# Kernel tuning notes

Measured on AMD Instinct MI355X. Metric: run time of the kernel, lower is better.

Reference implementation:

```python
import jax, jax.numpy as jnp
import numpy as np

B, C, H, W = 8, 64, 256, 256  # dim=64 -> chunks 32/16/8/8

def _dwconv3x3(x, w, b):
    # x: [N,Cg,H,W], w: [Cg,1,3,3] depthwise
    y = jax.lax.conv_general_dilated(
        x, w, window_strides=(1, 1), padding=((1, 1), (1, 1)),
        feature_group_count=x.shape[1],
        dimension_numbers=('NCHW', 'OIHW', 'NCHW'))
    return y + b[None, :, None, None]

def _maxpool4(x):
    # exact 4x4/stride-4 max pool == adaptive_max_pool2d when sizes divide
    return jax.lax.reduce_window(x, -jnp.inf, jax.lax.max,
                                 (1, 1, 4, 4), (1, 1, 4, 4), 'VALID')

def _upnearest(x, s):
    # nearest interpolate to (H,W) from (H/s,W/s) == repeat by s
    return jnp.repeat(jnp.repeat(x, s, axis=2), s, axis=3)

def setup_inputs() -> dict:
    key = jax.random.key(0)
    ks = jax.random.split(key, 11)
    sc = 0.05
    return {
        'x':  jax.random.normal(ks[0], (B, C, H, W), jnp.float32),
        'w1': jax.random.normal(ks[1], (32, 1, 3, 3), jnp.float32) * sc,
        'b1': jax.random.normal(ks[2], (32,), jnp.float32) * sc,
        'w2': jax.random.normal(ks[3], (16, 1, 3, 3), jnp.float32) * sc,
        'b2': jax.random.normal(ks[4], (16,), jnp.float32) * sc,
        'w3': jax.random.normal(ks[5], (8, 1, 3, 3), jnp.float32) * sc,
        'b3': jax.random.normal(ks[6], (8,), jnp.float32) * sc,
        'w4': jax.random.normal(ks[7], (8, 1, 3, 3), jnp.float32) * sc,
        'b4': jax.random.normal(ks[8], (8,), jnp.float32) * sc,
        'wa': jax.random.normal(ks[9], (64, 64), jnp.float32) * sc,  # 1x1 conv
        'ba': jax.random.normal(ks[10], (64,), jnp.float32) * sc,
    }

def reference(x, w1, b1, w2, b2, w3, b3, w4, b4, wa, ba):
    c = x.shape[1]
    xa, xb = x[:, : c // 2], x[:, c // 2 :]            # 32 / 32 channels
    x1 = _dwconv3x3(xa, w1, b1)                        # [B,32,H,W]
    p2 = _maxpool4(xb)                                 # [B,32,H/4,W/4]
    p2a, p2b = p2[:, :16], p2[:, 16:]
    x2 = _upnearest(_dwconv3x3(p2a, w2, b2), 4)        # [B,16,H,W]
    p3 = _maxpool4(p2b)                                # [B,16,H/16,W/16]
    p3a, p3b = p3[:, :8], p3[:, 8:]
    x3 = _upnearest(_dwconv3x3(p3a, w3, b3), 16)       # [B,8,H,W]
    p4 = _maxpool4(p3b)                                # [B,8,H/64,W/64]
    x4 = _upnearest(_dwconv3x3(p4, w4, b4), 64)        # [B,8,H,W]
    cat = jnp.concatenate([x1, x2, x3, x4], axis=1)    # [B,64,H,W]
    agg = jnp.einsum('oc,bchw->bohw', wa, cat) + ba[None, :, None, None]
    return jax.nn.gelu(agg, approximate=False) * x
```

## Files before the change

### kernel.cpp

```cpp
#include <hip/hip_runtime.h>
#include <math.h>

#define NB 8
#define NC 64
#define NH 256
#define NW 256

typedef short short8 __attribute__((ext_vector_type(8)));
typedef float f32x4 __attribute__((ext_vector_type(4)));

__device__ __forceinline__ unsigned short f2bf(float f) {
    unsigned int u = __float_as_uint(f);
    u += 0x7FFFu + ((u >> 16) & 1u);
    return (unsigned short)(u >> 16);
}

__device__ __forceinline__ int slot_of(int px, int g) {
    return g ^ (px & 7) ^ ((px >> 3) & 7);
}

__launch_bounds__(256)
__global__ void pyramid_kernel(const float* __restrict__ x,
                               const float* __restrict__ w2, const float* __restrict__ b2,
                               const float* __restrict__ w3, const float* __restrict__ b3,
                               const float* __restrict__ w4, const float* __restrict__ b4,
                               float* __restrict__ x2c, float* __restrict__ x3c,
                               float* __restrict__ x4c) {
    __shared__ float pl[64 * 65];
    __shared__ float pl2[16 * 17];
    __shared__ float pl3[16];

    const int tid = threadIdx.x;
    const int c = blockIdx.x & 31;
    const int b = blockIdx.x >> 5;
    const size_t plane = (size_t)NH * NW;
    const float* src = x + ((size_t)(b * 64 + 32 + c)) * plane;

#pragma unroll
    for (int i = 0; i < 16; ++i) {
        int o = tid + 256 * i;
        int pw = o & 63, ph = o >> 6;
        const float* s2 = src + (size_t)(ph * 4) * NW + pw * 4;
        float m = -INFINITY;
#pragma unroll
        for (int r = 0; r < 4; ++r) {
            float4 v = *reinterpret_cast<const float4*>(s2 + (size_t)r * NW);
            m = fmaxf(m, fmaxf(fmaxf(v.x, v.y), fmaxf(v.z, v.w)));
        }
        pl[ph * 65 + pw] = m;
    }
    __syncthreads();

    if (c < 16) {
        float* dst = x2c + ((size_t)(b * 16 + c)) * 4096;
        const float* wc = w2 + c * 9;
        float bb = b2[c];
#pragma unroll
        for (int i = 0; i < 16; ++i) {
            int o = tid + 256 * i;
            int pw = o & 63, ph = o >> 6;
            float acc = bb;
#pragma unroll
            for (int dy = -1; dy <= 1; ++dy) {
                int yy = ph + dy;
                if (yy < 0 || yy >= 64) continue;
#pragma unroll
                for (int dx = -1; dx <= 1; ++dx) {
                    int xx = pw + dx;
                    if (xx < 0 || xx >= 64) continue;
                    acc += pl[yy * 65 + xx] * wc[(dy + 1) * 3 + (dx + 1)];
                }
            }
            dst[o] = acc;
        }
    } else {
        {
            int pw = tid & 15, ph = tid >> 4;
            float m = -INFINITY;
#pragma unroll
            for (int r = 0; r < 4; ++r)
#pragma unroll
                for (int cc = 0; cc < 4; ++cc)
                    m = fmaxf(m, pl[(ph * 4 + r) * 65 + pw * 4 + cc]);
            pl2[ph * 17 + pw] = m;
        }
        __syncthreads();
        if (c < 24) {
            int pw = tid & 15, ph = tid >> 4;
            const float* wc = w3 + (c - 16) * 9;
            float acc = b3[c - 16];
#pragma unroll
            for (int dy = -1; dy <= 1; ++dy) {
                int yy = ph + dy;
                if (yy < 0 || yy >= 16) continue;
#pragma unroll
                for (int dx = -1; dx <= 1; ++dx) {
                    int xx = pw + dx;
                    if (xx < 0 || xx >= 16) continue;
                    acc += pl2[yy * 17 + xx] * wc[(dy + 1) * 3 + (dx + 1)];
                }
            }
            x3c[((size_t)(b * 8 + (c - 16))) * 256 + tid] = acc;
        } else {
            if (tid < 16) {
                int pw = tid & 3, ph = tid >> 2;
                float m = -INFINITY;
#pragma unroll
                for (int r = 0; r < 4; ++r)
#pragma unroll
                    for (int cc = 0; cc < 4; ++cc)
                        m = fmaxf(m, pl2[(ph * 4 + r) * 17 + pw * 4 + cc]);
                pl3[ph * 4 + pw] = m;
            }
            __syncthreads();
            if (tid < 16) {
                int pw = tid & 3, ph = tid >> 2;
                const float* wc = w4 + (c - 24) * 9;
                float acc = b4[c - 24];
#pragma unroll
                for (int dy = -1; dy <= 1; ++dy) {
                    int yy = ph + dy;
                    if (yy < 0 || yy >= 4) continue;
#pragma unroll
                    for (int dx = -1; dx <= 1; ++dx) {
                        int xx = pw + dx;
                        if (xx < 0 || xx >= 4) continue;
                        acc += pl3[yy * 4 + xx] * wc[(dy + 1) * 3 + (dx + 1)];
                    }
                }
                x4c[((size_t)(b * 8 + (c - 24))) * 16 + tid] = acc;
            }
        }
    }
}

__launch_bounds__(256)
__global__ void fused_main(const float* __restrict__ x,
                           const float* __restrict__ w1, const float* __restrict__ b1,
                           const float* __restrict__ x2c,
                           const float* __restrict__ x3c,
                           const float* __restrict__ x4c,
                           const float* __restrict__ wa, const float* __restrict__ ba,
                           float* __restrict__ out) {
    __shared__ __align__(16) unsigned short cat_lds[256 * 64];
    __shared__ __align__(16) unsigned short wa_lds[64 * 64];

    const int tid = threadIdx.x;
    const int q = tid & 63;
    const int cg = tid >> 6;
    const int h = blockIdx.x & 255;
    const int b = blockIdx.x >> 8;
    const size_t plane = (size_t)NH * NW;
    const float* xb = x + (size_t)b * NC * plane;

    {
        int r = tid >> 2;
        int g0 = (tid & 3) * 2;
#pragma unroll
        for (int gg = 0; gg < 2; ++gg) {
            int g = g0 + gg;
            const float* srcw = wa + r * 64 + g * 8;
            int4 pk;
            pk.x = (unsigned)f2bf(srcw[0]) | ((unsigned)f2bf(srcw[1]) << 16);
            pk.y = (unsigned)f2bf(srcw[2]) | ((unsigned)f2bf(srcw[3]) << 16);
            pk.z = (unsigned)f2bf(srcw[4]) | ((unsigned)f2bf(srcw[5]) << 16);
            pk.w = (unsigned)f2bf(srcw[6]) | ((unsigned)f2bf(srcw[7]) << 16);
            *reinterpret_cast<int4*>(&wa_lds[r * 64 + slot_of(r, g) * 8]) = pk;
        }
    }

    const bool hv0 = (h > 0), hv2 = (h < NH - 1);
    const int hm = hv0 ? h - 1 : h;
    const int hp = hv2 ? h + 1 : h;
    float conv[8][4];
#pragma unroll
    for (int j = 0; j < 8; ++j) {
        const int c = cg * 8 + j;
        const float* srcc = xb + (size_t)c * plane;
        float4 a0 = *reinterpret_cast<const float4*>(srcc + (size_t)hm * NW + 4 * q);
        float4 a1 = *reinterpret_cast<const float4*>(srcc + (size_t)h  * NW + 4 * q);
        float4 a2 = *reinterpret_cast<const float4*>(srcc + (size_t)hp * NW + 4 * q);
        const float* wc = w1 + c * 9;
        float k0 = hv0 ? wc[0] : 0.f, k1 = hv0 ? wc[1] : 0.f, k2 = hv0 ? wc[2] : 0.f;
        float k3 = wc[3], k4 = wc[4], k5 = wc[5];
        float k6 = hv2 ? wc[6] : 0.f, k7 = hv2 ? wc[7] : 0.f, k8 = hv2 ? wc[8] : 0.f;
        float p0 = __shfl_up(a0.w, 1), p1 = __shfl_up(a1.w, 1), p2 = __shfl_up(a2.w, 1);
        float n0 = __shfl_down(a0.x, 1), n1 = __shfl_down(a1.x, 1), n2 = __shfl_down(a2.x, 1);
        if (q == 0)  { p0 = 0.f; p1 = 0.f; p2 = 0.f; }
        if (q == 63) { n0 = 0.f; n1 = 0.f; n2 = 0.f; }
        float r0[6] = {p0, a0.x, a0.y, a0.z, a0.w, n0};
        float r1[6] = {p1, a1.x, a1.y, a1.z, a1.w, n1};
        float r2[6] = {p2, a2.x, a2.y, a2.z, a2.w, n2};
#pragma unroll
        for (int i = 0; i < 4; ++i) {
            conv[j][i] = k0 * r0[i] + k1 * r0[i + 1] + k2 * r0[i + 2]
                       + k3 * r1[i] + k4 * r1[i + 1] + k5 * r1[i + 2]
                       + k6 * r2[i] + k7 * r2[i + 1] + k8 * r2[i + 2]
                       + b1[c];
        }
    }
#pragma unroll
    for (int i = 0; i < 4; ++i) {
        int px = 4 * q + i;
        int4 pk;
        pk.x = (unsigned)f2bf(conv[0][i]) | ((unsigned)f2bf(conv[1][i]) << 16);
        pk.y = (unsigned)f2bf(conv[2][i]) | ((unsigned)f2bf(conv[3][i]) << 16);
        pk.z = (unsigned)f2bf(conv[4][i]) | ((unsigned)f2bf(conv[5][i]) << 16);
        pk.w = (unsigned)f2bf(conv[6][i]) | ((unsigned)f2bf(conv[7][i]) << 16);
        *reinterpret_cast<int4*>(&cat_lds[px * 64 + slot_of(px, cg) * 8]) = pk;
    }

    {
        float pv[8];
        const int h4 = h >> 2, h16 = h >> 4, h64 = h >> 6;
        if (cg == 0) {
#pragma unroll
            for (int j = 0; j < 8; ++j)
                pv[j] = x2c[(((size_t)b * 16 + j) * 64 + h4) * 64 + q];
        } else if (cg == 1) {
#pragma unroll
            for (int j = 0; j < 8; ++j)
                pv[j] = x2c[(((size_t)b * 16 + 8 + j) * 64 + h4) * 64 + q];
        } else if (cg == 2) {
#pragma unroll
            for (int j = 0; j < 8; ++j)
                pv[j] = x3c[(((size_t)b * 8 + j) * 16 + h16) * 16 + (q >> 2)];
        } else {
#pragma unroll
            for (int j = 0; j < 8; ++j)
                pv[j] = x4c[(((size_t)b * 8 + j) * 4 + h64) * 4 + (q >> 4)];
        }
        int4 pk;
        pk.x = (unsigned)f2bf(pv[0]) | ((unsigned)f2bf(pv[1]) << 16);
        pk.y = (unsigned)f2bf(pv[2]) | ((unsigned)f2bf(pv[3]) << 16);
        pk.z = (unsigned)f2bf(pv[4]) | ((unsigned)f2bf(pv[5]) << 16);
        pk.w = (unsigned)f2bf(pv[6]) | ((unsigned)f2bf(pv[7]) << 16);
#pragma unroll
        for (int i = 0; i < 4; ++i) {
            int px = 4 * q + i;
            *reinterpret_cast<int4*>(&cat_lds[px * 64 + slot_of(px, 4 + cg) * 8]) = pk;
        }
    }

    __syncthreads();

    const int lane = tid & 63;
    const int lr = lane & 15;
    const int lk = lane >> 4;
    const int pxb = cg * 64;

    short8 bfrag[4][2];
#pragma unroll
    for (int nt = 0; nt < 4; ++nt) {
        int px = pxb + nt * 16 + lr;
#pragma unroll
        for (int kt = 0; kt < 2; ++kt) {
            int g = kt * 4 + lk;
            bfrag[nt][kt] = *reinterpret_cast<const short8*>(
                &cat_lds[px * 64 + slot_of(px, g) * 8]);
        }
    }
    __syncthreads();

    const size_t outrow = (size_t)h * NW;

#pragma unroll
    for (int mt = 0; mt < 4; ++mt) {
        short8 afrag[2];
        int row = mt * 16 + lr;
#pragma unroll
        for (int kt = 0; kt < 2; ++kt) {
            int g = kt * 4 + lk;
            afrag[kt] = *reinterpret_cast<const short8*>(
                &wa_lds[row * 64 + slot_of(row, g) * 8]);
        }
        int obase = mt * 16 + lk * 4;
        float bs0 = ba[obase], bs1 = ba[obase + 1], bs2 = ba[obase + 2], bs3 = ba[obase + 3];
        f32x4 acc[4];
#pragma unroll
        for (int nt = 0; nt < 4; ++nt) {
            acc[nt][0] = bs0; acc[nt][1] = bs1; acc[nt][2] = bs2; acc[nt][3] = bs3;
        }
#pragma unroll
        for (int nt = 0; nt < 4; ++nt)
#pragma unroll
            for (int kt = 0; kt < 2; ++kt)
                acc[nt] = __builtin_amdgcn_mfma_f32_16x16x32_bf16(
                    afrag[kt], bfrag[nt][kt], acc[nt], 0, 0, 0);

        float* buf = reinterpret_cast<float*>(cat_lds) + (mt & 1) * 4096;
#pragma unroll
        for (int nt = 0; nt < 4; ++nt) {
            int px = pxb + nt * 16 + lr;
#pragma unroll
            for (int r = 0; r < 4; ++r) {
                float a = acc[nt][r];
                float gl = 0.5f * a * (1.0f + erff(a * 0.70710678118654752f));
                buf[(lk * 4 + r) * 256 + px] = gl;
            }
        }
        __syncthreads();

#pragma unroll
        for (int i = 0; i < 4; ++i) {
            int t2 = tid + 256 * i;
            int chLoc = t2 >> 6;
            int pq = t2 & 63;
            float4 gv = *reinterpret_cast<const float4*>(&buf[chLoc * 256 + pq * 4]);
            size_t off = ((size_t)(b * 64 + mt * 16 + chLoc)) * plane + outrow + pq * 4;
            float4 xv = *reinterpret_cast<const float4*>(&x[off]);
            float4 ov;
            ov.x = gv.x * xv.x; ov.y = gv.y * xv.y; ov.z = gv.z * xv.z; ov.w = gv.w * xv.w;
            *reinterpret_cast<float4*>(&out[off]) = ov;
        }
    }
}

extern "C" void kernel_launch(void* const* d_in, const int* in_sizes, int n_in,
                              void* d_out, int out_size, void* d_ws, size_t ws_size,
                              hipStream_t stream) {
    const float* x  = (const float*)d_in[0];
    const float* w1 = (const float*)d_in[1];
    const float* b1 = (const float*)d_in[2];
    const float* w2 = (const float*)d_in[3];
    const float* b2 = (const float*)d_in[4];
    const float* w3 = (const float*)d_in[5];
    const float* b3 = (const float*)d_in[6];
    const float* w4 = (const float*)d_in[7];
    const float* b4 = (const float*)d_in[8];
    const float* wa = (const float*)d_in[9];
    const float* ba = (const float*)d_in[10];
    float* out = (float*)d_out;

    float* ws  = (float*)d_ws;
    float* x2c = ws;
    float* x3c = x2c + 524288;
    float* x4c = x3c + 16384;

    pyramid_kernel<<<NB * 32, 256, 0, stream>>>(x, w2, b2, w3, b3, w4, b4,
                                                x2c, x3c, x4c);
    fused_main<<<NB * NH, 256, 0, stream>>>(x, w1, b1, x2c, x3c, x4c, wa, ba, out);
}
```

Before: 295.0 us.

## Widen pyramid blocks, prefetch x for gating, swizzle GELU buffer, reorder blocks

Moves the pyramid kernel from 256 to 1024 threads per block so its 256 blocks carry more parallelism, and guards the second-level work with tid<256. In the fused main kernel, blocks are reordered to batch-fastest, pyramid-branch loads are issued earlier, and the x values for the GELU gating are double-buffered in registers so the loads for the next channel tile overlap the current tile's store. An XOR swizzle on the LDS GELU buffer is meant to avoid bank conflicts. Register pressure rises from the prefetch buffers, and the larger pyramid blocks may reduce occupancy.

```diff
diff --git a/kernel.cpp b/kernel.cpp
--- a/kernel.cpp
+++ b/kernel.cpp
@@ -19,7 +19,7 @@
     return g ^ (px & 7) ^ ((px >> 3) & 7);
 }
 
-__launch_bounds__(256)
+__launch_bounds__(1024)
 __global__ void pyramid_kernel(const float* __restrict__ x,
                                const float* __restrict__ w2, const float* __restrict__ b2,
                                const float* __restrict__ w3, const float* __restrict__ b3,
@@ -37,8 +37,8 @@
     const float* src = x + ((size_t)(b * 64 + 32 + c)) * plane;
 
 #pragma unroll
-    for (int i = 0; i < 16; ++i) {
-        int o = tid + 256 * i;
+    for (int i = 0; i < 4; ++i) {
+        int o = tid + 1024 * i;
         int pw = o & 63, ph = o >> 6;
         const float* s2 = src + (size_t)(ph * 4) * NW + pw * 4;
         float m = -INFINITY;
@@ -56,8 +56,8 @@
         const float* wc = w2 + c * 9;
         float bb = b2[c];
 #pragma unroll
-        for (int i = 0; i < 16; ++i) {
-            int o = tid + 256 * i;
+        for (int i = 0; i < 4; ++i) {
+            int o = tid + 1024 * i;
             int pw = o & 63, ph = o >> 6;
             float acc = bb;
 #pragma unroll
@@ -74,7 +74,7 @@
             dst[o] = acc;
         }
     } else {
-        {
+        if (tid < 256) {
             int pw = tid & 15, ph = tid >> 4;
             float m = -INFINITY;
 #pragma unroll
@@ -86,21 +86,23 @@
         }
         __syncthreads();
         if (c < 24) {
-            int pw = tid & 15, ph = tid >> 4;
-            const float* wc = w3 + (c - 16) * 9;
-            float acc = b3[c - 16];
-#pragma unroll
-            for (int dy = -1; dy <= 1; ++dy) {
-                int yy = ph + dy;
-                if (yy < 0 || yy >= 16) continue;
-#pragma unroll
-                for (int dx = -1; dx <= 1; ++dx) {
-                    int xx = pw + dx;
-                    if (xx < 0 || xx >= 16) continue;
-                    acc += pl2[yy * 17 + xx] * wc[(dy + 1) * 3 + (dx + 1)];
+            if (tid < 256) {
+                int pw = tid & 15, ph = tid >> 4;
+                const float* wc = w3 + (c - 16) * 9;
+                float acc = b3[c - 16];
+#pragma unroll
+                for (int dy = -1; dy <= 1; ++dy) {
+                    int yy = ph + dy;
+                    if (yy < 0 || yy >= 16) continue;
+#pragma unroll
+                    for (int dx = -1; dx <= 1; ++dx) {
+                        int xx = pw + dx;
+                        if (xx < 0 || xx >= 16) continue;
+                        acc += pl2[yy * 17 + xx] * wc[(dy + 1) * 3 + (dx + 1)];
+                    }
                 }
-            }
-            x3c[((size_t)(b * 8 + (c - 16))) * 256 + tid] = acc;
+                x3c[((size_t)(b * 8 + (c - 16))) * 256 + tid] = acc;
+            }
         } else {
             if (tid < 16) {
                 int pw = tid & 3, ph = tid >> 2;
@@ -148,8 +150,9 @@
     const int tid = threadIdx.x;
     const int q = tid & 63;
     const int cg = tid >> 6;
-    const int h = blockIdx.x & 255;
-    const int b = blockIdx.x >> 8;
+    const int blk = blockIdx.x;
+    const int b = blk & 7;
+    const int h = blk >> 3;
     const size_t plane = (size_t)NH * NW;
     const float* xb = x + (size_t)b * NC * plane;
 
@@ -166,6 +169,28 @@
             pk.z = (unsigned)f2bf(srcw[4]) | ((unsigned)f2bf(srcw[5]) << 16);
             pk.w = (unsigned)f2bf(srcw[6]) | ((unsigned)f2bf(srcw[7]) << 16);
             *reinterpret_cast<int4*>(&wa_lds[r * 64 + slot_of(r, g) * 8]) = pk;
+        }
+    }
+
+    float pv[8];
+    {
+        const int h4 = h >> 2, h16 = h >> 4, h64 = h >> 6;
+        if (cg == 0) {
+#pragma unroll
+            for (int j = 0; j < 8; ++j)
+                pv[j] = x2c[(((size_t)b * 16 + j) * 64 + h4) * 64 + q];
+        } else if (cg == 1) {
+#pragma unroll
+            for (int j = 0; j < 8; ++j)
+                pv[j] = x2c[(((size_t)b * 16 + 8 + j) * 64 + h4) * 64 + q];
+        } else if (cg == 2) {
+#pragma unroll
+            for (int j = 0; j < 8; ++j)
+                pv[j] = x3c[(((size_t)b * 8 + j) * 16 + h16) * 16 + (q >> 2)];
+        } else {
+#pragma unroll
+            for (int j = 0; j < 8; ++j)
+                pv[j] = x4c[(((size_t)b * 8 + j) * 4 + h64) * 4 + (q >> 4)];
         }
     }
 
@@ -209,27 +234,7 @@
         pk.w = (unsigned)f2bf(conv[6][i]) | ((unsigned)f2bf(conv[7][i]) << 16);
         *reinterpret_cast<int4*>(&cat_lds[px * 64 + slot_of(px, cg) * 8]) = pk;
     }
-
     {
-        float pv[8];
-        const int h4 = h >> 2, h16 = h >> 4, h64 = h >> 6;
-        if (cg == 0) {
-#pragma unroll
-            for (int j = 0; j < 8; ++j)
-                pv[j] = x2c[(((size_t)b * 16 + j) * 64 + h4) * 64 + q];
-        } else if (cg == 1) {
-#pragma unroll
-            for (int j = 0; j < 8; ++j)
-                pv[j] = x2c[(((size_t)b * 16 + 8 + j) * 64 + h4) * 64 + q];
-        } else if (cg == 2) {
-#pragma unroll
-            for (int j = 0; j < 8; ++j)
-                pv[j] = x3c[(((size_t)b * 8 + j) * 16 + h16) * 16 + (q >> 2)];
-        } else {
-#pragma unroll
-            for (int j = 0; j < 8; ++j)
-                pv[j] = x4c[(((size_t)b * 8 + j) * 4 + h64) * 4 + (q >> 4)];
-        }
         int4 pk;
         pk.x = (unsigned)f2bf(pv[0]) | ((unsigned)f2bf(pv[1]) << 16);
         pk.y = (unsigned)f2bf(pv[2]) | ((unsigned)f2bf(pv[3]) << 16);
@@ -263,6 +268,15 @@
     __syncthreads();
 
     const size_t outrow = (size_t)h * NW;
+    size_t goff[4];
+#pragma unroll
+    for (int i = 0; i < 4; ++i)
+        goff[i] = ((size_t)(b * 64 + cg + 4 * i)) * plane + outrow + q * 4;
+
+    float4 xcur[4], xnxt[4];
+#pragma unroll
+    for (int i = 0; i < 4; ++i)
+        xcur[i] = *reinterpret_cast<const float4*>(&x[goff[i]]);
 
 #pragma unroll
     for (int mt = 0; mt < 4; ++mt) {
@@ -294,25 +308,34 @@
             int px = pxb + nt * 16 + lr;
 #pragma unroll
             for (int r = 0; r < 4; ++r) {
+                int rw = lk * 4 + r;
                 float a = acc[nt][r];
                 float gl = 0.5f * a * (1.0f + erff(a * 0.70710678118654752f));
-                buf[(lk * 4 + r) * 256 + px] = gl;
+                buf[rw * 256 + (px ^ ((rw & 7) << 2))] = gl;
             }
         }
         __syncthreads();
 
+        if (mt < 3) {
+#pragma unroll
+            for (int i = 0; i < 4; ++i)
+                xnxt[i] = *reinterpret_cast<const float4*>(
+                    &x[goff[i] + (size_t)((mt + 1) * 16) * plane]);
+        }
+
 #pragma unroll
         for (int i = 0; i < 4; ++i) {
-            int t2 = tid + 256 * i;
-            int chLoc = t2 >> 6;
-            int pq = t2 & 63;
-            float4 gv = *reinterpret_cast<const float4*>(&buf[chLoc * 256 + pq * 4]);
-            size_t off = ((size_t)(b * 64 + mt * 16 + chLoc)) * plane + outrow + pq * 4;
-            float4 xv = *reinterpret_cast<const float4*>(&x[off]);
+            int chLoc = cg + 4 * i;
+            float4 gv = *reinterpret_cast<const float4*>(
+                &buf[chLoc * 256 + ((q * 4) ^ ((chLoc & 7) << 2))]);
+            size_t off = goff[i] + (size_t)(mt * 16) * plane;
             float4 ov;
-            ov.x = gv.x * xv.x; ov.y = gv.y * xv.y; ov.z = gv.z * xv.z; ov.w = gv.w * xv.w;
+            ov.x = gv.x * xcur[i].x; ov.y = gv.y * xcur[i].y;
+            ov.z = gv.z * xcur[i].z; ov.w = gv.w * xcur[i].w;
             *reinterpret_cast<float4*>(&out[off]) = ov;
         }
+#pragma unroll
+        for (int i = 0; i < 4; ++i) xcur[i] = xnxt[i];
     }
 }
 
@@ -337,7 +360,7 @@
     float* x3c = x2c + 524288;
     float* x4c = x3c + 16384;
 
-    pyramid_kernel<<<NB * 32, 256, 0, stream>>>(x, w2, b2, w3, b3, w4, b4,
-                                                x2c, x3c, x4c);
+    pyramid_kernel<<<NB * 32, 1024, 0, stream>>>(x, w2, b2, w3, b3, w4, b4,
+                                                 x2c, x3c, x4c);
     fused_main<<<NB * NH, 256, 0, stream>>>(x, w1, b1, x2c, x3c, x4c, wa, ba, out);
 }
```

Measured after the change: 282.5 us. -4.2%, faster.
